# Kernel tuning notes

Hardware: AMD Instinct MI355X
Metric: run time of the kernel (lower is better)

The kernel has to match this reference:

```python
import jax, jax.numpy as jnp
import numpy as np

EPS = 1e-5
TAU_MAX = 1.0  # undefined global in source; assumed 1.0


def _conv4d(x, w, b, stride):
    # x: [N,C,T,X,Y,Z], w: [O,I,kt,kx,ky,kz], VALID padding (dense equivalent of strided Minkowski conv)
    dn = jax.lax.conv_dimension_numbers(x.shape, w.shape, ('NCTXYZ', 'OITXYZ', 'NCTXYZ'))
    y = jax.lax.conv_general_dilated(x, w, window_strides=stride, padding='VALID', dimension_numbers=dn)
    return y + b.reshape(1, -1, 1, 1, 1, 1)


def _bn(x, g, b, m, v):
    # inference-mode batchnorm over channel axis 1
    shape = (1, -1) + (1,) * (x.ndim - 2)
    return (x - m.reshape(shape)) * (g.reshape(shape) / jnp.sqrt(v.reshape(shape) + EPS)) + b.reshape(shape)


def setup_inputs() -> dict:
    key = jax.random.key(0)
    ks = jax.random.split(key, 32)
    f32 = jnp.float32
    d = {}
    d['x'] = jax.random.normal(ks[0], (4, 2, 6, 120, 120, 96), f32)
    d['jnt_pos'] = jax.random.normal(ks[1], (4, 6), f32)
    d['jnt_goal'] = jax.random.normal(ks[2], (4, 6), f32)
    # conv1: 2->64, k3 s3
    d['w1'] = jax.random.normal(ks[3], (64, 2, 3, 3, 3, 3), f32) * 0.05
    d['b1'] = jax.random.normal(ks[4], (64,), f32) * 0.05
    d['g1'] = jax.random.uniform(ks[5], (64,), f32, 0.5, 1.5)
    d['be1'] = jax.random.normal(ks[6], (64,), f32) * 0.05
    d['m1'] = jax.random.normal(ks[7], (64,), f32) * 0.05
    d['v1'] = jax.random.uniform(ks[8], (64,), f32, 0.5, 1.5)
    # conv2: 64->128, k2 s2
    d['w2'] = jax.random.normal(ks[9], (128, 64, 2, 2, 2, 2), f32) * 0.05
    d['b2'] = jax.random.normal(ks[10], (128,), f32) * 0.05
    d['g2'] = jax.random.uniform(ks[11], (128,), f32, 0.5, 1.5)
    d['be2'] = jax.random.normal(ks[12], (128,), f32) * 0.05
    d['m2'] = jax.random.normal(ks[13], (128,), f32) * 0.05
    d['v2'] = jax.random.uniform(ks[14], (128,), f32, 0.5, 1.5)
    # conv4: 128->256, k=(1,10,10,8) s=(1,10,10,8)
    d['w4'] = jax.random.normal(ks[15], (256, 128, 1, 10, 10, 8), f32) * 0.02
    d['b4'] = jax.random.normal(ks[16], (256,), f32) * 0.05
    # norm (BatchNorm1d(256))
    d['gn'] = jax.random.uniform(ks[17], (256,), f32, 0.5, 1.5)
    d['ben'] = jax.random.normal(ks[18], (256,), f32) * 0.05
    d['mn'] = jax.random.normal(ks[19], (256,), f32) * 0.05
    d['vn'] = jax.random.uniform(ks[20], (256,), f32, 0.5, 1.5)
    # linear: 256+12 -> 512, + BN
    d['wl'] = jax.random.normal(ks[21], (512, 268), f32) * 0.05
    d['bl'] = jax.random.normal(ks[22], (512,), f32) * 0.05
    d['gl'] = jax.random.uniform(ks[23], (512,), f32, 0.5, 1.5)
    d['bel'] = jax.random.normal(ks[24], (512,), f32) * 0.05
    d['ml'] = jax.random.normal(ks[25], (512,), f32) * 0.05
    d['vl'] = jax.random.uniform(ks[26], (512,), f32, 0.5, 1.5)
    # out: 512 -> 6
    d['wo'] = jax.random.normal(ks[27], (6, 512), f32) * 0.05
    d['bo'] = jax.random.normal(ks[28], (6,), f32) * 0.05
    return d


def reference(x, jnt_pos, jnt_goal, w1, b1, g1, be1, m1, v1, w2, b2, g2, be2, m2, v2,
              w4, b4, gn, ben, mn, vn, wl, bl, gl, bel, ml, vl, wo, bo):
    # pool1: max pool (1,2,2,2) stride (1,2,2,2)
    h = jax.lax.reduce_window(x, -jnp.inf, jax.lax.max,
                              window_dimensions=(1, 1, 1, 2, 2, 2),
                              window_strides=(1, 1, 1, 2, 2, 2), padding='VALID')
    h = jax.nn.relu(_bn(_conv4d(h, w1, b1, (3, 3, 3, 3)), g1, be1, m1, v1))
    h = jax.nn.relu(_bn(_conv4d(h, w2, b2, (2, 2, 2, 2)), g2, be2, m2, v2))
    h = _conv4d(h, w4, b4, (1, 10, 10, 8))          # [B,256,1,1,1,1]
    h = jnp.max(h, axis=(2, 3, 4, 5))               # global max pool -> [B,256]
    # to_dense_tnsr is an identity scatter (row b <- row b) after global pooling
    h = jax.nn.relu(_bn(h, gn, ben, mn, vn))
    # dropout eval-mode = identity
    h = jnp.concatenate([jnt_pos, jnt_goal, h], axis=1)   # [B,268]
    h = jax.nn.relu(_bn(h @ wl.T + bl, gl, bel, ml, vl))  # [B,512]
    return jnp.tanh(h @ wo.T + bo) * TAU_MAX              # [B,6]
```

## Files before the change

kernel.cpp:

```cpp
#include <hip/hip_runtime.h>
#include <hip/hip_bf16.h>


typedef float f32x4_t __attribute__((ext_vector_type(4)));

__device__ __forceinline__ float wave_reduce(float v) {
#pragma unroll
    for (int off = 32; off > 0; off >>= 1) v += __shfl_down(v, off);
    return v;
}

__global__ void k_prep(const float* __restrict__ w1, const float* __restrict__ w2,
                       float* __restrict__ w1t, float* __restrict__ w2t) {
    int tid = blockIdx.x * blockDim.x + threadIdx.x;
    int nthr = gridDim.x * blockDim.x;
    for (int i = tid; i < 64 * 162; i += nthr) {
        int o = i / 162, t = i % 162;
        w1t[t * 64 + o] = w1[i];
    }
    for (int i = tid; i < 128 * 1024; i += nthr) {
        int o = i / 1024, t = i % 1024;
        w2t[t * 128 + o] = w2[i];
    }
}

__global__ __launch_bounds__(256) void k_conv1(
    const float* __restrict__ x, const float* __restrict__ w1t,
    const float* __restrict__ b1, const float* __restrict__ g1,
    const float* __restrict__ be1, const float* __restrict__ m1,
    const float* __restrict__ v1, float* __restrict__ y1) {
    int bid = blockIdx.x;
    int yo = bid % 20; bid /= 20;
    int xo = bid % 20; bid /= 20;
    int t  = bid % 2;  bid /= 2;
    int n  = bid;

    __shared__ float pooled[2592];
    int tid = threadIdx.x;

    for (int task = tid; task < 1296; task += 256) {
        int q = task % 24; int r = task / 24;
        int py = r % 3; r /= 3;
        int px = r % 3; r /= 3;
        int tp = r % 3; int c = r / 3;
        const float* base = x + ((((size_t)n * 2 + c) * 6 + 3 * t + tp) * 120 + 6 * xo + 2 * px) * 11520
                              + (size_t)(6 * yo + 2 * py) * 96 + 4 * q;
        float4 v00 = *(const float4*)(base);
        float4 v01 = *(const float4*)(base + 96);
        float4 v10 = *(const float4*)(base + 11520);
        float4 v11 = *(const float4*)(base + 11520 + 96);
        float p0 = fmaxf(fmaxf(fmaxf(v00.x, v00.y), fmaxf(v01.x, v01.y)),
                         fmaxf(fmaxf(v10.x, v10.y), fmaxf(v11.x, v11.y)));
        float p1 = fmaxf(fmaxf(fmaxf(v00.z, v00.w), fmaxf(v01.z, v01.w)),
                         fmaxf(fmaxf(v10.z, v10.w), fmaxf(v11.z, v11.w)));
        int row = ((c * 3 + tp) * 3 + px) * 3 + py;
        int z0 = 2 * q, z1 = 2 * q + 1;
        pooled[row * 48 + (z0 % 3) * 16 + z0 / 3] = p0;
        pooled[row * 48 + (z1 % 3) * 16 + z1 / 3] = p1;
    }
    __syncthreads();

    int o  = tid & 63;
    int zg = tid >> 6;
    float acc[4] = {0.f, 0.f, 0.f, 0.f};
    for (int row = 0; row < 54; ++row) {
        const float* pr = &pooled[row * 48 + zg * 4];
#pragma unroll
        for (int kz = 0; kz < 3; ++kz) {
            float w = w1t[(row * 3 + kz) * 64 + o];
            float4 pv = *(const float4*)(pr + kz * 16);
            acc[0] = fmaf(w, pv.x, acc[0]);
            acc[1] = fmaf(w, pv.y, acc[1]);
            acc[2] = fmaf(w, pv.z, acc[2]);
            acc[3] = fmaf(w, pv.w, acc[3]);
        }
    }
    float s  = g1[o] * rsqrtf(v1[o] + 1e-5f);
    float sh = be1[o] + (b1[o] - m1[o]) * s;
    size_t obase = ((((size_t)n * 64 + o) * 2 + t) * 20 + xo) * 320 + (size_t)yo * 16 + zg * 4;
    float4 outv;
    outv.x = fmaxf(acc[0] * s + sh, 0.f);
    outv.y = fmaxf(acc[1] * s + sh, 0.f);
    outv.z = fmaxf(acc[2] * s + sh, 0.f);
    outv.w = fmaxf(acc[3] * s + sh, 0.f);
    *(float4*)&y1[obase] = outv;
}

__global__ __launch_bounds__(512) void k_conv2(
    const float* __restrict__ y1, const float* __restrict__ w2t,
    const float* __restrict__ b2, const float* __restrict__ g2,
    const float* __restrict__ be2, const float* __restrict__ m2,
    const float* __restrict__ v2, float* __restrict__ y2) {
    int bid = blockIdx.x;
    int yo = bid % 10; bid /= 10;
    int xo = bid % 10; bid /= 10;
    int n  = bid;

    __shared__ float in2t[8192];
    __shared__ float red[8192];
    int tid = threadIdx.x;
#pragma unroll
    for (int it = 0; it < 4; ++it) {
        int task = tid + it * 512;
        int a = task & 3; int row = task >> 2;
        int ky = row & 1, kx = (row >> 1) & 1, kt = (row >> 2) & 1, c = row >> 3;
        const float* src = y1 + ((((size_t)n * 64 + c) * 2 + kt) * 20 + 2 * xo + kx) * 320
                              + (size_t)(2 * yo + ky) * 16 + 4 * a;
        float4 v = *(const float4*)src;
        *(float2*)&in2t[row * 8 + 2 * a]        = make_float2(v.x, v.z);
        *(float2*)&in2t[4096 + row * 8 + 2 * a] = make_float2(v.y, v.w);
    }
    __syncthreads();

    int o2 = tid & 63;
    int ks = tid >> 6;
    float acc[2][8];
#pragma unroll
    for (int a = 0; a < 2; ++a)
#pragma unroll
        for (int b = 0; b < 8; ++b) acc[a][b] = 0.f;

    for (int rr = 0; rr < 64; ++rr) {
        int row = ks * 64 + rr;
#pragma unroll
        for (int kz = 0; kz < 2; ++kz) {
            float2 w = *(const float2*)&w2t[(row * 2 + kz) * 128 + 2 * o2];
            float4 p0 = *(const float4*)&in2t[kz * 4096 + row * 8];
            float4 p1 = *(const float4*)&in2t[kz * 4096 + row * 8 + 4];
            acc[0][0] = fmaf(w.x, p0.x, acc[0][0]);
            acc[0][1] = fmaf(w.x, p0.y, acc[0][1]);
            acc[0][2] = fmaf(w.x, p0.z, acc[0][2]);
            acc[0][3] = fmaf(w.x, p0.w, acc[0][3]);
            acc[0][4] = fmaf(w.x, p1.x, acc[0][4]);
            acc[0][5] = fmaf(w.x, p1.y, acc[0][5]);
            acc[0][6] = fmaf(w.x, p1.z, acc[0][6]);
            acc[0][7] = fmaf(w.x, p1.w, acc[0][7]);
            acc[1][0] = fmaf(w.y, p0.x, acc[1][0]);
            acc[1][1] = fmaf(w.y, p0.y, acc[1][1]);
            acc[1][2] = fmaf(w.y, p0.z, acc[1][2]);
            acc[1][3] = fmaf(w.y, p0.w, acc[1][3]);
            acc[1][4] = fmaf(w.y, p1.x, acc[1][4]);
            acc[1][5] = fmaf(w.y, p1.y, acc[1][5]);
            acc[1][6] = fmaf(w.y, p1.z, acc[1][6]);
            acc[1][7] = fmaf(w.y, p1.w, acc[1][7]);
        }
    }
#pragma unroll
    for (int a = 0; a < 2; ++a)
#pragma unroll
        for (int b = 0; b < 8; ++b) red[ks * 1024 + o2 * 16 + a * 8 + b] = acc[a][b];
    __syncthreads();

#pragma unroll
    for (int e = tid; e < 1024; e += 512) {
        float v = 0.f;
#pragma unroll
        for (int k = 0; k < 8; ++k) v += red[k * 1024 + e];
        int o2e = e >> 4, i = e & 15;
        int o = o2e * 2 + (i >> 3), zo = i & 7;
        float s  = g2[o] * rsqrtf(v2[o] + 1e-5f);
        float sh = be2[o] + (b2[o] - m2[o]) * s;
        y2[(((size_t)n * 128 + o) * 10 + xo) * 80 + (size_t)yo * 8 + zo] = fmaxf(v * s + sh, 0.f);
    }
}

__global__ __launch_bounds__(256) void k_conv4(
    const float* __restrict__ y2, const float* __restrict__ w4,
    float* __restrict__ part) {
    int oc = blockIdx.x & 63;
    int kc = blockIdx.x >> 6;
    int tid = threadIdx.x;
    const float4* y2v = (const float4*)y2;
    const f32x4_t* w4v = (const f32x4_t*)w4;
    float acc[4][4];
#pragma unroll
    for (int a = 0; a < 4; ++a)
#pragma unroll
        for (int b = 0; b < 4; ++b) acc[a][b] = 0.f;

    int base = kc * 2560;
#pragma unroll 2
    for (int i = 0; i < 10; ++i) {
        int f4 = base + i * 256 + tid;
        float4 a0 = y2v[f4];
        float4 a1 = y2v[25600 + f4];
        float4 a2 = y2v[51200 + f4];
        float4 a3 = y2v[76800 + f4];
#pragma unroll
        for (int oo = 0; oo < 4; ++oo) {
            f32x4_t w = __builtin_nontemporal_load(&w4v[(size_t)(oc * 4 + oo) * 25600 + f4]);
            acc[oo][0] = fmaf(w.x, a0.x, fmaf(w.y, a0.y, fmaf(w.z, a0.z, fmaf(w.w, a0.w, acc[oo][0]))));
            acc[oo][1] = fmaf(w.x, a1.x, fmaf(w.y, a1.y, fmaf(w.z, a1.z, fmaf(w.w, a1.w, acc[oo][1]))));
            acc[oo][2] = fmaf(w.x, a2.x, fmaf(w.y, a2.y, fmaf(w.z, a2.z, fmaf(w.w, a2.w, acc[oo][2]))));
            acc[oo][3] = fmaf(w.x, a3.x, fmaf(w.y, a3.y, fmaf(w.z, a3.z, fmaf(w.w, a3.w, acc[oo][3]))));
        }
    }
    __shared__ float red[4][16];
    int wave = tid >> 6, lane = tid & 63;
#pragma unroll
    for (int oo = 0; oo < 4; ++oo)
#pragma unroll
        for (int nn = 0; nn < 4; ++nn) {
            float v = wave_reduce(acc[oo][nn]);
            if (lane == 0) red[wave][oo * 4 + nn] = v;
        }
    __syncthreads();
    if (tid < 16) {
        float sum = red[0][tid] + red[1][tid] + red[2][tid] + red[3][tid];
        part[(size_t)blockIdx.x * 16 + tid] = sum;
    }
}

__global__ __launch_bounds__(256) void k_lin1(
    const float* __restrict__ part, const float* __restrict__ b4,
    const float* __restrict__ gn, const float* __restrict__ ben,
    const float* __restrict__ mn, const float* __restrict__ vn,
    const float* __restrict__ jp, const float* __restrict__ jg,
    const float* __restrict__ wl, const float* __restrict__ bl,
    const float* __restrict__ gl, const float* __restrict__ bel,
    const float* __restrict__ ml, const float* __restrict__ vl,
    float* __restrict__ h2) {
    __shared__ float feat[4 * 268];
    int tid = threadIdx.x;
    {
        int o = tid;
        int oc = o >> 2, oo = o & 3;
        float s  = gn[o] * rsqrtf(vn[o] + 1e-5f);
        float sh = ben[o] + (b4[o] - mn[o]) * s;
#pragma unroll
        for (int nn = 0; nn < 4; ++nn) {
            float acc = 0.f;
#pragma unroll
            for (int kc = 0; kc < 10; ++kc) acc += part[(kc * 64 + oc) * 16 + oo * 4 + nn];
            feat[nn * 268 + 12 + o] = fmaxf(acc * s + sh, 0.f);
        }
        if (o < 24) {
            int nn = o / 6, j = o % 6;
            feat[nn * 268 + j] = jp[o];
            feat[nn * 268 + 6 + j] = jg[o];
        }
    }
    __syncthreads();

    int wave = tid >> 6, lane = tid & 63;
    int j = blockIdx.x * 4 + wave;
    const float* wr = wl + (size_t)j * 268;
    float acc[4] = {0.f, 0.f, 0.f, 0.f};
    for (int k = lane; k < 268; k += 64) {
        float w = wr[k];
#pragma unroll
        for (int nn = 0; nn < 4; ++nn) acc[nn] = fmaf(w, feat[nn * 268 + k], acc[nn]);
    }
#pragma unroll
    for (int nn = 0; nn < 4; ++nn) acc[nn] = wave_reduce(acc[nn]);
    if (lane == 0) {
        float s  = gl[j] * rsqrtf(vl[j] + 1e-5f);
        float sh = bel[j] + (bl[j] - ml[j]) * s;
#pragma unroll
        for (int nn = 0; nn < 4; ++nn) h2[nn * 512 + j] = fmaxf(acc[nn] * s + sh, 0.f);
    }
}

__global__ void k_lin2(const float* __restrict__ h2, const float* __restrict__ wo,
                       const float* __restrict__ bo, float* __restrict__ out) {
    int wave = threadIdx.x >> 6, lane = threadIdx.x & 63;
    int n = wave;
    float hv[8];
#pragma unroll
    for (int i = 0; i < 8; ++i) hv[i] = h2[n * 512 + i * 64 + lane];
    for (int o = 0; o < 6; ++o) {
        float acc = 0.f;
#pragma unroll
        for (int i = 0; i < 8; ++i) acc = fmaf(hv[i], wo[o * 512 + i * 64 + lane], acc);
        acc = wave_reduce(acc);
        if (lane == 0) out[n * 6 + o] = tanhf(acc + bo[o]);
    }
}

extern "C" void kernel_launch(void* const* d_in, const int* in_sizes, int n_in,
                              void* d_out, int out_size, void* d_ws, size_t ws_size,
                              hipStream_t stream) {
    const float* x   = (const float*)d_in[0];
    const float* jp  = (const float*)d_in[1];
    const float* jg  = (const float*)d_in[2];
    const float* w1  = (const float*)d_in[3];
    const float* b1  = (const float*)d_in[4];
    const float* g1  = (const float*)d_in[5];
    const float* be1 = (const float*)d_in[6];
    const float* m1  = (const float*)d_in[7];
    const float* v1  = (const float*)d_in[8];
    const float* w2  = (const float*)d_in[9];
    const float* b2  = (const float*)d_in[10];
    const float* g2  = (const float*)d_in[11];
    const float* be2 = (const float*)d_in[12];
    const float* m2  = (const float*)d_in[13];
    const float* v2  = (const float*)d_in[14];
    const float* w4  = (const float*)d_in[15];
    const float* b4  = (const float*)d_in[16];
    const float* gn  = (const float*)d_in[17];
    const float* ben = (const float*)d_in[18];
    const float* mn  = (const float*)d_in[19];
    const float* vn  = (const float*)d_in[20];
    const float* wl  = (const float*)d_in[21];
    const float* bl  = (const float*)d_in[22];
    const float* gl  = (const float*)d_in[23];
    const float* bel = (const float*)d_in[24];
    const float* ml  = (const float*)d_in[25];
    const float* vl  = (const float*)d_in[26];
    const float* wo  = (const float*)d_in[27];
    const float* bo  = (const float*)d_in[28];
    float* out = (float*)d_out;

    float* ws   = (float*)d_ws;
    float* w1t  = ws;
    float* w2t  = ws + 10368;
    float* y1   = ws + 141440;
    float* y2   = ws + 3418240;
    float* part = ws + 3827840;
    float* h2   = ws + 3838080;

    k_prep<<<64, 256, 0, stream>>>(w1, w2, w1t, w2t);
    k_conv1<<<3200, 256, 0, stream>>>(x, w1t, b1, g1, be1, m1, v1, y1);
    k_conv2<<<400, 512, 0, stream>>>(y1, w2t, b2, g2, be2, m2, v2, y2);
    k_conv4<<<640, 256, 0, stream>>>(y2, w4, part);
    k_lin1<<<128, 256, 0, stream>>>(part, b4, gn, ben, mn, vn, jp, jg,
                                    wl, bl, gl, bel, ml, vl, h2);
    k_lin2<<<1, 256, 0, stream>>>(h2, wo, bo, out);
}
```

Baseline: 124.0 us.

## Fuse w2 transpose into conv1, widen conv1 per-thread work, merge head kernels

The w1 transpose now writes coalesced, and the w2 transpose runs in 64 extra blocks appended to the conv1 grid, so it no longer needs its own launch. conv1 drops to 128 threads per block, each computing 8 z outputs, which doubles reuse of every loaded weight. lin1 and lin2 are merged into a single-block head kernel that keeps h2 in shared memory, removing one launch and a global round-trip. The risk is that the single-block lin1, with one thread per output row doing strided float4 weight loads, is less parallel than the old 128-block version.

```diff
diff --git a/kernel.cpp b/kernel.cpp
--- a/kernel.cpp
+++ b/kernel.cpp
@@ -10,25 +10,28 @@
     return v;
 }
 
-__global__ void k_prep(const float* __restrict__ w1, const float* __restrict__ w2,
-                       float* __restrict__ w1t, float* __restrict__ w2t) {
-    int tid = blockIdx.x * blockDim.x + threadIdx.x;
-    int nthr = gridDim.x * blockDim.x;
-    for (int i = tid; i < 64 * 162; i += nthr) {
-        int o = i / 162, t = i % 162;
-        w1t[t * 64 + o] = w1[i];
-    }
-    for (int i = tid; i < 128 * 1024; i += nthr) {
-        int o = i / 1024, t = i % 1024;
-        w2t[t * 128 + o] = w2[i];
-    }
-}
-
-__global__ __launch_bounds__(256) void k_conv1(
+__global__ void k_prep_w1(const float* __restrict__ w1, float* __restrict__ w1t) {
+    for (int i = blockIdx.x * 256 + threadIdx.x; i < 64 * 162; i += gridDim.x * 256) {
+        int t = i >> 6, o = i & 63;
+        w1t[i] = w1[o * 162 + t];
+    }
+}
+
+__global__ __launch_bounds__(128) void k_conv1(
     const float* __restrict__ x, const float* __restrict__ w1t,
     const float* __restrict__ b1, const float* __restrict__ g1,
     const float* __restrict__ be1, const float* __restrict__ m1,
-    const float* __restrict__ v1, float* __restrict__ y1) {
+    const float* __restrict__ v1, float* __restrict__ y1,
+    const float* __restrict__ w2, float* __restrict__ w2t) {
+    int tid = threadIdx.x;
+    if (blockIdx.x >= 3200) {
+        int bw = blockIdx.x - 3200;
+        for (int i = bw * 128 + tid; i < 128 * 1024; i += 64 * 128) {
+            int t = i >> 7, o = i & 127;
+            w2t[i] = w2[o * 1024 + t];
+        }
+        return;
+    }
     int bid = blockIdx.x;
     int yo = bid % 20; bid /= 20;
     int xo = bid % 20; bid /= 20;
@@ -36,9 +39,8 @@
     int n  = bid;
 
     __shared__ float pooled[2592];
-    int tid = threadIdx.x;
-
-    for (int task = tid; task < 1296; task += 256) {
+
+    for (int task = tid; task < 1296; task += 128) {
         int q = task % 24; int r = task / 24;
         int py = r % 3; r /= 3;
         int px = r % 3; r /= 3;
@@ -62,28 +64,41 @@
 
     int o  = tid & 63;
     int zg = tid >> 6;
-    float acc[4] = {0.f, 0.f, 0.f, 0.f};
+    float acc[8];
+#pragma unroll
+    for (int j = 0; j < 8; ++j) acc[j] = 0.f;
+
     for (int row = 0; row < 54; ++row) {
-        const float* pr = &pooled[row * 48 + zg * 4];
+        const float* pr = &pooled[row * 48 + zg * 8];
 #pragma unroll
         for (int kz = 0; kz < 3; ++kz) {
             float w = w1t[(row * 3 + kz) * 64 + o];
-            float4 pv = *(const float4*)(pr + kz * 16);
-            acc[0] = fmaf(w, pv.x, acc[0]);
-            acc[1] = fmaf(w, pv.y, acc[1]);
-            acc[2] = fmaf(w, pv.z, acc[2]);
-            acc[3] = fmaf(w, pv.w, acc[3]);
+            float4 p0 = *(const float4*)(pr + kz * 16);
+            float4 p1 = *(const float4*)(pr + kz * 16 + 4);
+            acc[0] = fmaf(w, p0.x, acc[0]);
+            acc[1] = fmaf(w, p0.y, acc[1]);
+            acc[2] = fmaf(w, p0.z, acc[2]);
+            acc[3] = fmaf(w, p0.w, acc[3]);
+            acc[4] = fmaf(w, p1.x, acc[4]);
+            acc[5] = fmaf(w, p1.y, acc[5]);
+            acc[6] = fmaf(w, p1.z, acc[6]);
+            acc[7] = fmaf(w, p1.w, acc[7]);
         }
     }
     float s  = g1[o] * rsqrtf(v1[o] + 1e-5f);
     float sh = be1[o] + (b1[o] - m1[o]) * s;
-    size_t obase = ((((size_t)n * 64 + o) * 2 + t) * 20 + xo) * 320 + (size_t)yo * 16 + zg * 4;
-    float4 outv;
-    outv.x = fmaxf(acc[0] * s + sh, 0.f);
-    outv.y = fmaxf(acc[1] * s + sh, 0.f);
-    outv.z = fmaxf(acc[2] * s + sh, 0.f);
-    outv.w = fmaxf(acc[3] * s + sh, 0.f);
-    *(float4*)&y1[obase] = outv;
+    size_t obase = ((((size_t)n * 64 + o) * 2 + t) * 20 + xo) * 320 + (size_t)yo * 16 + zg * 8;
+    float4 o0, o1;
+    o0.x = fmaxf(acc[0] * s + sh, 0.f);
+    o0.y = fmaxf(acc[1] * s + sh, 0.f);
+    o0.z = fmaxf(acc[2] * s + sh, 0.f);
+    o0.w = fmaxf(acc[3] * s + sh, 0.f);
+    o1.x = fmaxf(acc[4] * s + sh, 0.f);
+    o1.y = fmaxf(acc[5] * s + sh, 0.f);
+    o1.z = fmaxf(acc[6] * s + sh, 0.f);
+    o1.w = fmaxf(acc[7] * s + sh, 0.f);
+    *(float4*)&y1[obase]     = o0;
+    *(float4*)&y1[obase + 4] = o1;
 }
 
 __global__ __launch_bounds__(512) void k_conv2(
@@ -211,7 +226,7 @@
     }
 }
 
-__global__ __launch_bounds__(256) void k_lin1(
+__global__ __launch_bounds__(512) void k_head(
     const float* __restrict__ part, const float* __restrict__ b4,
     const float* __restrict__ gn, const float* __restrict__ ben,
     const float* __restrict__ mn, const float* __restrict__ vn,
@@ -219,21 +234,26 @@
     const float* __restrict__ wl, const float* __restrict__ bl,
     const float* __restrict__ gl, const float* __restrict__ bel,
     const float* __restrict__ ml, const float* __restrict__ vl,
-    float* __restrict__ h2) {
+    const float* __restrict__ wo, const float* __restrict__ bo,
+    float* __restrict__ out) {
     __shared__ float feat[4 * 268];
+    __shared__ float h2l[4 * 512];
     int tid = threadIdx.x;
-    {
+
+    if (tid < 256) {
         int o = tid;
-        int oc = o >> 2, oo = o & 3;
+        float a0 = 0.f, a1 = 0.f, a2 = 0.f, a3 = 0.f;
+#pragma unroll
+        for (int kc = 0; kc < 10; ++kc) {
+            float4 p = *(const float4*)&part[kc * 1024 + o * 4];
+            a0 += p.x; a1 += p.y; a2 += p.z; a3 += p.w;
+        }
         float s  = gn[o] * rsqrtf(vn[o] + 1e-5f);
         float sh = ben[o] + (b4[o] - mn[o]) * s;
-#pragma unroll
-        for (int nn = 0; nn < 4; ++nn) {
-            float acc = 0.f;
-#pragma unroll
-            for (int kc = 0; kc < 10; ++kc) acc += part[(kc * 64 + oc) * 16 + oo * 4 + nn];
-            feat[nn * 268 + 12 + o] = fmaxf(acc * s + sh, 0.f);
-        }
+        feat[0 * 268 + 12 + o] = fmaxf(a0 * s + sh, 0.f);
+        feat[1 * 268 + 12 + o] = fmaxf(a1 * s + sh, 0.f);
+        feat[2 * 268 + 12 + o] = fmaxf(a2 * s + sh, 0.f);
+        feat[3 * 268 + 12 + o] = fmaxf(a3 * s + sh, 0.f);
         if (o < 24) {
             int nn = o / 6, j = o % 6;
             feat[nn * 268 + j] = jp[o];
@@ -242,38 +262,38 @@
     }
     __syncthreads();
 
-    int wave = tid >> 6, lane = tid & 63;
-    int j = blockIdx.x * 4 + wave;
-    const float* wr = wl + (size_t)j * 268;
-    float acc[4] = {0.f, 0.f, 0.f, 0.f};
-    for (int k = lane; k < 268; k += 64) {
-        float w = wr[k];
-#pragma unroll
-        for (int nn = 0; nn < 4; ++nn) acc[nn] = fmaf(w, feat[nn * 268 + k], acc[nn]);
-    }
-#pragma unroll
-    for (int nn = 0; nn < 4; ++nn) acc[nn] = wave_reduce(acc[nn]);
-    if (lane == 0) {
+    {
+        int j = tid;
+        const float4* wr4 = (const float4*)(wl + (size_t)j * 268);
+        float acc[4] = {0.f, 0.f, 0.f, 0.f};
+        for (int k4 = 0; k4 < 67; ++k4) {
+            float4 w = wr4[k4];
+#pragma unroll
+            for (int nn = 0; nn < 4; ++nn) {
+                float4 f = *(const float4*)&feat[nn * 268 + k4 * 4];
+                acc[nn] = fmaf(w.x, f.x, fmaf(w.y, f.y, fmaf(w.z, f.z, fmaf(w.w, f.w, acc[nn]))));
+            }
+        }
         float s  = gl[j] * rsqrtf(vl[j] + 1e-5f);
         float sh = bel[j] + (bl[j] - ml[j]) * s;
 #pragma unroll
-        for (int nn = 0; nn < 4; ++nn) h2[nn * 512 + j] = fmaxf(acc[nn] * s + sh, 0.f);
-    }
-}
-
-__global__ void k_lin2(const float* __restrict__ h2, const float* __restrict__ wo,
-                       const float* __restrict__ bo, float* __restrict__ out) {
-    int wave = threadIdx.x >> 6, lane = threadIdx.x & 63;
-    int n = wave;
-    float hv[8];
-#pragma unroll
-    for (int i = 0; i < 8; ++i) hv[i] = h2[n * 512 + i * 64 + lane];
-    for (int o = 0; o < 6; ++o) {
-        float acc = 0.f;
-#pragma unroll
-        for (int i = 0; i < 8; ++i) acc = fmaf(hv[i], wo[o * 512 + i * 64 + lane], acc);
-        acc = wave_reduce(acc);
-        if (lane == 0) out[n * 6 + o] = tanhf(acc + bo[o]);
+        for (int nn = 0; nn < 4; ++nn) h2l[nn * 512 + j] = fmaxf(acc[nn] * s + sh, 0.f);
+    }
+    __syncthreads();
+
+    if (tid < 256) {
+        int wave = tid >> 6, lane = tid & 63;
+        int n = wave;
+        float hv[8];
+#pragma unroll
+        for (int i = 0; i < 8; ++i) hv[i] = h2l[n * 512 + i * 64 + lane];
+        for (int o = 0; o < 6; ++o) {
+            float acc = 0.f;
+#pragma unroll
+            for (int i = 0; i < 8; ++i) acc = fmaf(hv[i], wo[o * 512 + i * 64 + lane], acc);
+            acc = wave_reduce(acc);
+            if (lane == 0) out[n * 6 + o] = tanhf(acc + bo[o]);
+        }
     }
 }
 
@@ -317,13 +337,11 @@
     float* y1   = ws + 141440;
     float* y2   = ws + 3418240;
     float* part = ws + 3827840;
-    float* h2   = ws + 3838080;
-
-    k_prep<<<64, 256, 0, stream>>>(w1, w2, w1t, w2t);
-    k_conv1<<<3200, 256, 0, stream>>>(x, w1t, b1, g1, be1, m1, v1, y1);
+
+    k_prep_w1<<<16, 256, 0, stream>>>(w1, w1t);
+    k_conv1<<<3264, 128, 0, stream>>>(x, w1t, b1, g1, be1, m1, v1, y1, w2, w2t);
     k_conv2<<<400, 512, 0, stream>>>(y1, w2t, b2, g2, be2, m2, v2, y2);
     k_conv4<<<640, 256, 0, stream>>>(y2, w4, part);
-    k_lin1<<<128, 256, 0, stream>>>(part, b4, gn, ben, mn, vn, jp, jg,
-                                    wl, bl, gl, bel, ml, vl, h2);
-    k_lin2<<<1, 256, 0, stream>>>(h2, wo, bo, out);
-}
+    k_head<<<1, 512, 0, stream>>>(part, b4, gn, ben, mn, vn, jp, jg,
+                                  wl, bl, gl, bel, ml, vl, wo, bo, out);
+}
```

Result: slower. 156.8 us (+26.5%).
